# Optimization experiments

Hardware: AMD Instinct MI355X
Metric: run time of the kernel (lower is better)

Reference implementation:

```python
import jax, jax.numpy as jnp
import numpy as np

DEPTH, DIM, HEADS, DIM_HEAD, MLP = 6, 768, 12, 64, 3072
INNER = HEADS * DIM_HEAD  # 768
EPS = 1e-5


def _layernorm(x, w, b):
    m = jnp.mean(x, axis=-1, keepdims=True)
    v = jnp.mean((x - m) ** 2, axis=-1, keepdims=True)
    return (x - m) * jax.lax.rsqrt(v + EPS) * w + b


def setup_inputs() -> dict:
    key = jax.random.key(0)
    ks = jax.random.split(key, 12)
    s = 0.02
    return {
        "x": jax.random.normal(ks[0], (4, 1024, DIM), dtype=jnp.float32),
        "ln1_w": jnp.ones((DEPTH, DIM), jnp.float32),
        "ln1_b": jnp.zeros((DEPTH, DIM), jnp.float32),
        "w_qkv": jax.random.normal(ks[1], (DEPTH, DIM, 3 * INNER), jnp.float32) * s,
        "w_o": jax.random.normal(ks[2], (DEPTH, INNER, DIM), jnp.float32) * s,
        "b_o": jnp.zeros((DEPTH, DIM), jnp.float32),
        "ln2_w": jnp.ones((DEPTH, DIM), jnp.float32),
        "ln2_b": jnp.zeros((DEPTH, DIM), jnp.float32),
        "w1": jax.random.normal(ks[3], (DEPTH, DIM, MLP), jnp.float32) * s,
        "b1": jnp.zeros((DEPTH, MLP), jnp.float32),
        "w2": jax.random.normal(ks[4], (DEPTH, MLP, DIM), jnp.float32) * s,
        "b2": jnp.zeros((DEPTH, DIM), jnp.float32),
    }


def _forward(x, ln1_w, ln1_b, w_qkv, w_o, b_o, ln2_w, ln2_b, w1, b1, w2, b2):
    scale = DIM_HEAD ** -0.5
    b, n, _ = x.shape

    def block(x, p):
        l1w, l1b, wqkv, wo, bo, l2w, l2b, W1, B1, W2, B2 = p
        # --- attention (pre-norm); dropout/droppath are identity in eval ---
        h = _layernorm(x, l1w, l1b)
        qkv = h @ wqkv                                   # [b, n, 3*inner]
        q, k, v = jnp.split(qkv, 3, axis=-1)
        q = q.reshape(b, n, HEADS, DIM_HEAD).transpose(0, 2, 1, 3)
        k = k.reshape(b, n, HEADS, DIM_HEAD).transpose(0, 2, 1, 3)
        v = v.reshape(b, n, HEADS, DIM_HEAD).transpose(0, 2, 1, 3)
        dots = jnp.einsum('bhid,bhjd->bhij', q, k) * scale   # [b, h, n, n]
        attn = jax.nn.softmax(dots, axis=-1)
        out = jnp.einsum('bhij,bhjd->bhid', attn, v)
        out = out.transpose(0, 2, 1, 3).reshape(b, n, INNER)
        x = x + out @ wo + bo
        # --- feed-forward (pre-norm), exact GELU like torch default ---
        h = _layernorm(x, l2w, l2b)
        x = x + jax.nn.gelu(h @ W1 + B1, approximate=False) @ W2 + B2
        return x, None

    x, _ = jax.lax.scan(block, x, (ln1_w, ln1_b, w_qkv, w_o, b_o,
                                   ln2_w, ln2_b, w1, b1, w2, b2))
    return x


def reference(x, ln1_w, ln1_b, w_qkv, w_o, b_o, ln2_w, ln2_b, w1, b1, w2, b2):
    return _forward(x, ln1_w, ln1_b, w_qkv, w_o, b_o, ln2_w, ln2_b, w1, b1, w2, b2)
```

## Files before the change

kernel.cpp:

```cpp
#include <hip/hip_runtime.h>
#include <cmath>
#include <cstdint>

typedef __bf16 bf16_t;
typedef __bf16 bf16x8 __attribute__((ext_vector_type(8)));
typedef __bf16 bf16x4 __attribute__((ext_vector_type(4)));
typedef float  f32x4  __attribute__((ext_vector_type(4)));

#define DEPTH 6
#define DIM   768
#define HEADS 12
#define DH    64
#define MLPD  3072
#define SEQ   1024
#define BATCH 4
#define MTOT  (BATCH*SEQ)
#define QKVN  2304

static __device__ __forceinline__ bf16x8 ld8(const bf16_t* p) {
    return *(const bf16x8*)p;
}

typedef const __attribute__((address_space(1))) unsigned int gas_u32;
typedef __attribute__((address_space(3))) unsigned int las_u32;
static __device__ __forceinline__ void gload16(const bf16_t* g, bf16_t* l) {
    __builtin_amdgcn_global_load_lds((gas_u32*)g, (las_u32*)l, 16, 0, 0);
}

__global__ __launch_bounds__(256) void tcvt_kernel(const float* __restrict__ in,
                                                   bf16_t* __restrict__ out,
                                                   int K, int N) {
    __shared__ float ts[32][33];
    int n0 = blockIdx.x * 32, k0 = blockIdx.y * 32;
    size_t base = (size_t)blockIdx.z * K * N;
    int tx = threadIdx.x & 31, ty = threadIdx.x >> 5;
    #pragma unroll
    for (int r = 0; r < 32; r += 8)
        ts[ty + r][tx] = in[base + (size_t)(k0 + ty + r) * N + n0 + tx];
    __syncthreads();
    #pragma unroll
    for (int r = 0; r < 32; r += 8)
        out[base + (size_t)(n0 + ty + r) * K + k0 + tx] = (bf16_t)ts[tx][ty + r];
}

__global__ __launch_bounds__(256) void lnr_kernel(float* __restrict__ x,
                                                  const float* __restrict__ P,
                                                  int nslices,
                                                  const float* __restrict__ bias,
                                                  const float* __restrict__ w,
                                                  const float* __restrict__ b,
                                                  bf16_t* __restrict__ h,
                                                  int writeLN) {
    int lane = threadIdx.x & 63;
    int row = blockIdx.x * 4 + (threadIdx.x >> 6);
    float4* xr = (float4*)(x + (size_t)row * DIM);
    float4 v0 = xr[lane], v1 = xr[lane + 64], v2 = xr[lane + 128];
    if (nslices) {
        const float4* bi = (const float4*)bias;
        float4 c0 = bi[lane], c1 = bi[lane + 64], c2 = bi[lane + 128];
        v0.x += c0.x; v0.y += c0.y; v0.z += c0.z; v0.w += c0.w;
        v1.x += c1.x; v1.y += c1.y; v1.z += c1.z; v1.w += c1.w;
        v2.x += c2.x; v2.y += c2.y; v2.z += c2.z; v2.w += c2.w;
        for (int s = 0; s < nslices; s++) {
            const float4* pr = (const float4*)(P + (size_t)s * MTOT * DIM
                                                 + (size_t)row * DIM);
            float4 p0 = pr[lane], p1 = pr[lane + 64], p2 = pr[lane + 128];
            v0.x += p0.x; v0.y += p0.y; v0.z += p0.z; v0.w += p0.w;
            v1.x += p1.x; v1.y += p1.y; v1.z += p1.z; v1.w += p1.w;
            v2.x += p2.x; v2.y += p2.y; v2.z += p2.z; v2.w += p2.w;
        }
        xr[lane] = v0; xr[lane + 64] = v1; xr[lane + 128] = v2;
    }
    float s = v0.x + v0.y + v0.z + v0.w + v1.x + v1.y + v1.z + v1.w
            + v2.x + v2.y + v2.z + v2.w;
    float q = v0.x * v0.x + v0.y * v0.y + v0.z * v0.z + v0.w * v0.w
            + v1.x * v1.x + v1.y * v1.y + v1.z * v1.z + v1.w * v1.w
            + v2.x * v2.x + v2.y * v2.y + v2.z * v2.z + v2.w * v2.w;
    #pragma unroll
    for (int off = 32; off > 0; off >>= 1) {
        s += __shfl_xor(s, off);
        q += __shfl_xor(q, off);
    }
    float mean = s * (1.0f / DIM);
    float rstd = rsqrtf(q * (1.0f / DIM) - mean * mean + 1e-5f);
    if (writeLN) {
        const float4* w4 = (const float4*)w;
        const float4* b4 = (const float4*)b;
        bf16_t* hr = h + (size_t)row * DIM;
        float4 vv[3] = {v0, v1, v2};
        #pragma unroll
        for (int k = 0; k < 3; k++) {
            float4 wv = w4[lane + 64 * k], bv = b4[lane + 64 * k];
            bf16x4 o;
            o[0] = (bf16_t)((vv[k].x - mean) * rstd * wv.x + bv.x);
            o[1] = (bf16_t)((vv[k].y - mean) * rstd * wv.y + bv.y);
            o[2] = (bf16_t)((vv[k].z - mean) * rstd * wv.z + bv.z);
            o[3] = (bf16_t)((vv[k].w - mean) * rstd * wv.w + bv.w);
            *(bf16x4*)&hr[(lane + 64 * k) * 4] = o;
        }
    }
}

template <int EPI>
static __device__ __forceinline__ void gemm_body(const bf16_t* __restrict__ A,
                                                 const bf16_t* __restrict__ Bt,
                                                 const float* __restrict__ bias,
                                                 bf16_t* __restrict__ Cb,
                                                 float* __restrict__ Cf,
                                                 bf16_t* __restrict__ Vt,
                                                 int N, int K, int klen) {
    __shared__ __align__(16) bf16_t As[2][256 * 32];
    __shared__ __align__(16) bf16_t Bs[2][64 * 32];
    int t = threadIdx.x;
    int NX = gridDim.x;
    int flat = blockIdx.y * NX + blockIdx.x;
    int jj = flat >> 3;
    int bxs = jj % NX;
    int bys = (flat & 7) + ((jj / NX) << 3);
    int m0 = bys * 256, n0 = bxs * 64;
    int kz = blockIdx.z;
    int kbeg = kz * klen;
    int lane = t & 63, l16 = lane & 15, quad = lane >> 4;
    int wv = t >> 6;
    int wm = wv >> 1, wn = wv & 1;
    f32x4 acc[4][2] = {};

    int sr = lane >> 2;
    int sc = ((lane & 3) ^ ((lane >> 3) & 3)) * 8;
    const bf16_t* gA0 = A  + (size_t)(m0 + wv * 32 + sr) * K + sc;
    const bf16_t* gA1 = gA0 + (size_t)16 * K;
    const bf16_t* gB0 = Bt + (size_t)(n0 + (wv & 3) * 16 + sr) * K + sc;
    bf16_t* lA0 = &As[0][(wv * 32) * 32];
    bf16_t* lA1 = &As[0][(wv * 32 + 16) * 32];
    bf16_t* lB0 = &Bs[0][((wv & 3) * 16) * 32];
    constexpr int bufA = 256 * 32;
    constexpr int bufB = 64 * 32;

    auto stage = [&](int buf, int k0) {
        gload16(gA0 + k0, lA0 + buf * bufA);
        gload16(gA1 + k0, lA1 + buf * bufA);
        if (wv < 4) gload16(gB0 + k0, lB0 + buf * bufB);
    };

    int nIt = klen >> 5;
    stage(0, kbeg);
    int posA = (quad ^ ((l16 >> 1) & 3)) * 8;

    for (int it = 0; it < nIt; it++) {
        __syncthreads();
        if (it + 1 < nIt) stage((it + 1) & 1, kbeg + (it + 1) * 32);
        const bf16_t* as = As[it & 1];
        const bf16_t* bs = Bs[it & 1];
        bf16x8 af[4], bfr[2];
        #pragma unroll
        for (int i = 0; i < 4; i++)
            af[i] = ld8(&as[(wm * 64 + i * 16 + l16) * 32 + posA]);
        #pragma unroll
        for (int j = 0; j < 2; j++)
            bfr[j] = ld8(&bs[(wn * 32 + j * 16 + l16) * 32 + posA]);
        #pragma unroll
        for (int i = 0; i < 4; i++)
            #pragma unroll
            for (int j = 0; j < 2; j++)
                acc[i][j] = __builtin_amdgcn_mfma_f32_16x16x32_bf16(af[i], bfr[j], acc[i][j], 0, 0, 0);
    }

    if constexpr (EPI == 0) {
        if (n0 >= 1536) {
            int b = m0 >> 10;
            #pragma unroll
            for (int i = 0; i < 4; i++) {
                int n = (m0 & 1023) + wm * 64 + i * 16 + quad * 4;
                #pragma unroll
                for (int j = 0; j < 2; j++) {
                    int hc = n0 + wn * 32 + j * 16 + l16 - 1536;
                    int hh = hc >> 6, d = hc & 63;
                    bf16x4 ov;
                    #pragma unroll
                    for (int r = 0; r < 4; r++) ov[r] = (bf16_t)acc[i][j][r];
                    *(bf16x4*)&Vt[(((size_t)b * HEADS + hh) * 64 + d) * SEQ + n] = ov;
                }
            }
            return;
        }
    }
    #pragma unroll
    for (int i = 0; i < 4; i++) {
        int grow = m0 + wm * 64 + i * 16 + quad * 4;
        #pragma unroll
        for (int j = 0; j < 2; j++) {
            int gcol = n0 + wn * 32 + j * 16 + l16;
            float bv = 0.0f;
            if constexpr (EPI == 1) bv = bias[gcol];
            #pragma unroll
            for (int r = 0; r < 4; r++) {
                size_t idx = (size_t)(grow + r) * N + gcol;
                float v = acc[i][j][r];
                if constexpr (EPI == 0) {
                    Cb[idx] = (bf16_t)v;
                } else if constexpr (EPI == 1) {
                    v += bv;
                    v = 0.5f * v * (1.0f + erff(v * 0.70710678118654752f));
                    Cb[idx] = (bf16_t)v;
                } else {
                    Cf[(size_t)kz * MTOT * N + idx] = v;
                }
            }
        }
    }
}

__global__ __launch_bounds__(512) void qkv_gemm(const bf16_t* __restrict__ A,
                                                const bf16_t* __restrict__ Bt,
                                                bf16_t* __restrict__ Cb,
                                                bf16_t* __restrict__ Vt) {
    gemm_body<0>(A, Bt, nullptr, Cb, nullptr, Vt, QKVN, DIM, DIM);
}
__global__ __launch_bounds__(512) void proj_gemm(const bf16_t* __restrict__ A,
                                                 const bf16_t* __restrict__ Bt,
                                                 float* __restrict__ Cf) {
    gemm_body<2>(A, Bt, nullptr, nullptr, Cf, nullptr, DIM, DIM, 384);
}
__global__ __launch_bounds__(512) void mlp1_gemm(const bf16_t* __restrict__ A,
                                                 const bf16_t* __restrict__ Bt,
                                                 const float* __restrict__ bias,
                                                 bf16_t* __restrict__ Cb) {
    gemm_body<1>(A, Bt, bias, Cb, nullptr, nullptr, MLPD, DIM, DIM);
}
__global__ __launch_bounds__(512) void mlp2_gemm(const bf16_t* __restrict__ A,
                                                 const bf16_t* __restrict__ Bt,
                                                 float* __restrict__ Cf) {
    gemm_body<2>(A, Bt, nullptr, nullptr, Cf, nullptr, DIM, MLPD, 768);
}

__global__ __launch_bounds__(256) void attn_kernel(const bf16_t* __restrict__ qkv,
                                                   const bf16_t* __restrict__ vt,
                                                   bf16_t* __restrict__ out) {
    int flat = (blockIdx.z * gridDim.y + blockIdx.y) * gridDim.x + blockIdx.x;
    int jj = flat >> 3;
    int qt = jj & 15;
    int bh = (flat & 7) + ((jj >> 4) << 3);
    int h = bh % HEADS, b = bh / HEADS;
    int t = threadIdx.x;
    int wv = t >> 6, lane = t & 63, l16 = lane & 15, quad = lane >> 4;
    const float LOG2E = 1.44269504f;
    int qw0 = qt * 64 + wv * 16;

    __shared__ __align__(16) bf16_t Ks[2][64 * 64];
    __shared__ __align__(16) bf16_t Vs[2][64 * 64];
    __shared__ __align__(16) bf16_t Pa[4][16 * 72];
    bf16_t* P = Pa[wv];

    size_t bS = (size_t)b * SEQ;
    const bf16_t* qrow = qkv + (bS + qw0 + l16) * QKVN + h * 64;
    bf16x8 qf0 = ld8(qrow + quad * 8);
    bf16x8 qf1 = ld8(qrow + 32 + quad * 8);

    float m = -3e38f, l = 0.0f;
    f32x4 o[4] = {};

    const bf16_t* kbase = qkv + bS * QKVN + 768 + h * 64;
    const bf16_t* vbase = vt + ((size_t)(b * HEADS + h) * 64) * SEQ;

    int ar = lane >> 3;
    int ac = ((lane & 7) ^ ar) * 8;
    int i0 = wv * 2, i1 = wv * 2 + 1;
    const bf16_t* gK0 = kbase + (size_t)(i0 * 8 + ar) * QKVN + ac;
    const bf16_t* gK1 = kbase + (size_t)(i1 * 8 + ar) * QKVN + ac;
    const bf16_t* gV0 = vbase + (size_t)(i0 * 8 + ar) * SEQ + ac;
    const bf16_t* gV1 = vbase + (size_t)(i1 * 8 + ar) * SEQ + ac;

    auto stage = [&](int buf, int kb) {
        gload16(gK0 + (size_t)kb * QKVN, &Ks[buf][i0 * 8 * 64]);
        gload16(gK1 + (size_t)kb * QKVN, &Ks[buf][i1 * 8 * 64]);
        gload16(gV0 + kb, &Vs[buf][i0 * 8 * 64]);
        gload16(gV1 + kb, &Vs[buf][i1 * 8 * 64]);
    };

    stage(0, 0);
    int p0 = (quad ^ (l16 & 7)) * 8;
    int p1 = ((quad + 4) ^ (l16 & 7)) * 8;

    for (int it = 0; it < SEQ / 64; it++) {
        __syncthreads();
        if (it + 1 < SEQ / 64) stage((it + 1) & 1, (it + 1) * 64);
        const bf16_t* ks = Ks[it & 1];
        const bf16_t* vs = Vs[it & 1];

        f32x4 s[4];
        #pragma unroll
        for (int tt = 0; tt < 4; tt++) {
            const bf16_t* kr = &ks[(tt * 16 + l16) * 64];
            f32x4 z = {};
            z = __builtin_amdgcn_mfma_f32_16x16x32_bf16(ld8(kr + p0), qf0, z, 0, 0, 0);
            z = __builtin_amdgcn_mfma_f32_16x16x32_bf16(ld8(kr + p1), qf1, z, 0, 0, 0);
            s[tt] = z;
        }
        float mx = -3e38f;
        #pragma unroll
        for (int tt = 0; tt < 4; tt++)
            #pragma unroll
            for (int r = 0; r < 4; r++) {
                s[tt][r] *= 0.125f;
                mx = fmaxf(mx, s[tt][r]);
            }
        mx = fmaxf(mx, __shfl_xor(mx, 16));
        mx = fmaxf(mx, __shfl_xor(mx, 32));
        float mn = fmaxf(m, mx);
        float alpha = exp2f((m - mn) * LOG2E);
        m = mn;
        float nb = mn * LOG2E;
        float rs = 0.0f;
        #pragma unroll
        for (int tt = 0; tt < 4; tt++) {
            bf16x4 pkt;
            #pragma unroll
            for (int r = 0; r < 4; r++) {
                float p = exp2f(fmaf(s[tt][r], LOG2E, -nb));
                rs += p;
                pkt[r] = (bf16_t)p;
            }
            *(bf16x4*)&P[l16 * 72 + tt * 16 + quad * 4] = pkt;
        }
        l = l * alpha + rs;
        #pragma unroll
        for (int jt = 0; jt < 4; jt++) o[jt] *= alpha;
        asm volatile("s_waitcnt lgkmcnt(0)" ::: "memory");
        bf16x8 pf0 = ld8(&P[l16 * 72 + quad * 8]);
        bf16x8 pf1 = ld8(&P[l16 * 72 + 32 + quad * 8]);
        #pragma unroll
        for (int jt = 0; jt < 4; jt++) {
            const bf16_t* vr = &vs[(jt * 16 + l16) * 64];
            o[jt] = __builtin_amdgcn_mfma_f32_16x16x32_bf16(ld8(vr + p0), pf0, o[jt], 0, 0, 0);
            o[jt] = __builtin_amdgcn_mfma_f32_16x16x32_bf16(ld8(vr + p1), pf1, o[jt], 0, 0, 0);
        }
    }

    l += __shfl_xor(l, 16);
    l += __shfl_xor(l, 32);
    float inv = 1.0f / l;
    bf16_t* orow = out + (bS + qw0 + l16) * DIM + h * 64;
    #pragma unroll
    for (int jt = 0; jt < 4; jt++) {
        bf16x4 ov;
        #pragma unroll
        for (int r = 0; r < 4; r++) ov[r] = (bf16_t)(o[jt][r] * inv);
        *(bf16x4*)&orow[jt * 16 + quad * 4] = ov;
    }
}

extern "C" void kernel_launch(void* const* d_in, const int* in_sizes, int n_in,
                              void* d_out, int out_size, void* d_ws, size_t ws_size,
                              hipStream_t stream) {
    const float* x     = (const float*)d_in[0];
    const float* ln1_w = (const float*)d_in[1];
    const float* ln1_b = (const float*)d_in[2];
    const float* w_qkv = (const float*)d_in[3];
    const float* w_o   = (const float*)d_in[4];
    const float* b_o   = (const float*)d_in[5];
    const float* ln2_w = (const float*)d_in[6];
    const float* ln2_b = (const float*)d_in[7];
    const float* w1    = (const float*)d_in[8];
    const float* b1    = (const float*)d_in[9];
    const float* w2    = (const float*)d_in[10];
    const float* b2    = (const float*)d_in[11];
    float* out = (float*)d_out;

    char* ws = (char*)d_ws;
    size_t off = 0;
    auto alloc = [&](size_t bytes) -> char* {
        char* p = ws + off;
        off += (bytes + 255) & ~(size_t)255;
        return p;
    };
    bf16_t* wqkv_t = (bf16_t*)alloc((size_t)DEPTH * DIM * QKVN * 2);
    bf16_t* wo_t   = (bf16_t*)alloc((size_t)DEPTH * DIM * DIM * 2);
    bf16_t* w1_t   = (bf16_t*)alloc((size_t)DEPTH * DIM * MLPD * 2);
    bf16_t* w2_t   = (bf16_t*)alloc((size_t)DEPTH * MLPD * DIM * 2);
    bf16_t* hbuf   = (bf16_t*)alloc((size_t)MTOT * DIM * 2);
    bf16_t* qkvb   = (bf16_t*)alloc((size_t)MTOT * QKVN * 2);
    bf16_t* vtb    = (bf16_t*)alloc((size_t)BATCH * HEADS * 64 * SEQ * 2);
    bf16_t* aob    = (bf16_t*)alloc((size_t)MTOT * DIM * 2);
    bf16_t* midb   = (bf16_t*)alloc((size_t)MTOT * MLPD * 2);
    float*  Pm     = (float*)alloc((size_t)4 * MTOT * DIM * 4);
    float*  Pp     = (float*)qkvb;
    if (off > ws_size) return;

    tcvt_kernel<<<dim3(QKVN / 32, DIM / 32, DEPTH), 256, 0, stream>>>(w_qkv, wqkv_t, DIM, QKVN);
    tcvt_kernel<<<dim3(DIM / 32,  DIM / 32, DEPTH), 256, 0, stream>>>(w_o,   wo_t,   DIM, DIM);
    tcvt_kernel<<<dim3(MLPD / 32, DIM / 32, DEPTH), 256, 0, stream>>>(w1,    w1_t,   DIM, MLPD);
    tcvt_kernel<<<dim3(DIM / 32, MLPD / 32, DEPTH), 256, 0, stream>>>(w2,    w2_t,   MLPD, DIM);

    hipMemcpyAsync(out, x, (size_t)MTOT * DIM * 4, hipMemcpyDeviceToDevice, stream);

    lnr_kernel<<<MTOT / 4, 256, 0, stream>>>(out, nullptr, 0, nullptr,
                                             ln1_w, ln1_b, hbuf, 1);

    for (int L = 0; L < DEPTH; L++) {
        qkv_gemm<<<dim3(QKVN / 64, MTOT / 256, 1), 512, 0, stream>>>(
            hbuf, wqkv_t + (size_t)L * DIM * QKVN, qkvb, vtb);
        attn_kernel<<<dim3(SEQ / 64, HEADS, BATCH), 256, 0, stream>>>(qkvb, vtb, aob);
        proj_gemm<<<dim3(DIM / 64, MTOT / 256, 2), 512, 0, stream>>>(
            aob, wo_t + (size_t)L * DIM * DIM, Pp);
        lnr_kernel<<<MTOT / 4, 256, 0, stream>>>(out, Pp, 2, b_o + L * DIM,
                                                 ln2_w + L * DIM, ln2_b + L * DIM,
                                                 hbuf, 1);
        mlp1_gemm<<<dim3(MLPD / 64, MTOT / 256, 1), 512, 0, stream>>>(
            hbuf, w1_t + (size_t)L * DIM * MLPD, b1 + L * MLPD, midb);
        mlp2_gemm<<<dim3(DIM / 64, MTOT / 256, 4), 512, 0, stream>>>(
            midb, w2_t + (size_t)L * MLPD * DIM, Pm);
        if (L < DEPTH - 1) {
            lnr_kernel<<<MTOT / 4, 256, 0, stream>>>(out, Pm, 4, b2 + L * DIM,
                                                     ln1_w + (L + 1) * DIM,
                                                     ln1_b + (L + 1) * DIM, hbuf, 1);
        } else {
            lnr_kernel<<<MTOT / 4, 256, 0, stream>>>(out, Pm, 4, b2 + L * DIM,
                                                     nullptr, nullptr, nullptr, 0);
        }
    }
}
```

Baseline: 1.291 ms.

## Retile GEMMs to 128x64 blocks with 64-wide K stage and 4 waves

The shared GEMM body moves from 256x64 tiles with 8 waves and a K step of 32 to 128x64 tiles with 4 waves and a K step of 64. Each wave now does two MFMA sub-steps per barrier, and the LDS XOR swizzle is redone for 64-element rows. The aim is to halve the number of barriers and global-load rounds per K, double the block count, and lower per-block LDS and thread count so more blocks fit per CU. In exchange, each block reuses less data across M, so more global traffic goes to re-reading B.

```diff
diff --git a/kernel.cpp b/kernel.cpp
--- a/kernel.cpp
+++ b/kernel.cpp
@@ -109,15 +109,15 @@
                                                  float* __restrict__ Cf,
                                                  bf16_t* __restrict__ Vt,
                                                  int N, int K, int klen) {
-    __shared__ __align__(16) bf16_t As[2][256 * 32];
-    __shared__ __align__(16) bf16_t Bs[2][64 * 32];
+    __shared__ __align__(16) bf16_t As[2][128 * 64];
+    __shared__ __align__(16) bf16_t Bs[2][64 * 64];
     int t = threadIdx.x;
     int NX = gridDim.x;
     int flat = blockIdx.y * NX + blockIdx.x;
     int jj = flat >> 3;
     int bxs = jj % NX;
     int bys = (flat & 7) + ((jj / NX) << 3);
-    int m0 = bys * 256, n0 = bxs * 64;
+    int m0 = bys * 128, n0 = bxs * 64;
     int kz = blockIdx.z;
     int kbeg = kz * klen;
     int lane = t & 63, l16 = lane & 15, quad = lane >> 4;
@@ -125,44 +125,49 @@
     int wm = wv >> 1, wn = wv & 1;
     f32x4 acc[4][2] = {};
 
-    int sr = lane >> 2;
-    int sc = ((lane & 3) ^ ((lane >> 3) & 3)) * 8;
-    const bf16_t* gA0 = A  + (size_t)(m0 + wv * 32 + sr) * K + sc;
-    const bf16_t* gA1 = gA0 + (size_t)16 * K;
-    const bf16_t* gB0 = Bt + (size_t)(n0 + (wv & 3) * 16 + sr) * K + sc;
-    bf16_t* lA0 = &As[0][(wv * 32) * 32];
-    bf16_t* lA1 = &As[0][(wv * 32 + 16) * 32];
-    bf16_t* lB0 = &Bs[0][((wv & 3) * 16) * 32];
-    constexpr int bufA = 256 * 32;
-    constexpr int bufB = 64 * 32;
+    int ar = lane >> 3;
+    int ac = ((lane & 7) ^ ar) * 8;
+    const bf16_t* gA = A  + (size_t)(m0 + wv * 32 + ar) * K + ac;
+    const bf16_t* gB = Bt + (size_t)(n0 + wv * 16 + ar) * K + ac;
+    bf16_t* lA = &As[0][(wv * 32) * 64];
+    bf16_t* lB = &Bs[0][(wv * 16) * 64];
+    constexpr int bufA = 128 * 64;
+    constexpr int bufB = 64 * 64;
 
     auto stage = [&](int buf, int k0) {
-        gload16(gA0 + k0, lA0 + buf * bufA);
-        gload16(gA1 + k0, lA1 + buf * bufA);
-        if (wv < 4) gload16(gB0 + k0, lB0 + buf * bufB);
+        #pragma unroll
+        for (int i = 0; i < 4; i++)
+            gload16(gA + (size_t)(i * 8) * K + k0, lA + buf * bufA + i * 8 * 64);
+        #pragma unroll
+        for (int i = 0; i < 2; i++)
+            gload16(gB + (size_t)(i * 8) * K + k0, lB + buf * bufB + i * 8 * 64);
     };
 
-    int nIt = klen >> 5;
+    int nIt = klen >> 6;
     stage(0, kbeg);
-    int posA = (quad ^ ((l16 >> 1) & 3)) * 8;
+    int rk = l16 & 7;
 
     for (int it = 0; it < nIt; it++) {
         __syncthreads();
-        if (it + 1 < nIt) stage((it + 1) & 1, kbeg + (it + 1) * 32);
+        if (it + 1 < nIt) stage((it + 1) & 1, kbeg + (it + 1) * 64);
         const bf16_t* as = As[it & 1];
         const bf16_t* bs = Bs[it & 1];
-        bf16x8 af[4], bfr[2];
-        #pragma unroll
-        for (int i = 0; i < 4; i++)
-            af[i] = ld8(&as[(wm * 64 + i * 16 + l16) * 32 + posA]);
-        #pragma unroll
-        for (int j = 0; j < 2; j++)
-            bfr[j] = ld8(&bs[(wn * 32 + j * 16 + l16) * 32 + posA]);
-        #pragma unroll
-        for (int i = 0; i < 4; i++)
+        #pragma unroll
+        for (int kk = 0; kk < 2; kk++) {
+            int pos = ((kk * 4 + quad) ^ rk) * 8;
+            bf16x8 af[4], bfr[2];
+            #pragma unroll
+            for (int i = 0; i < 4; i++)
+                af[i] = ld8(&as[(wm * 64 + i * 16 + l16) * 64 + pos]);
             #pragma unroll
             for (int j = 0; j < 2; j++)
-                acc[i][j] = __builtin_amdgcn_mfma_f32_16x16x32_bf16(af[i], bfr[j], acc[i][j], 0, 0, 0);
+                bfr[j] = ld8(&bs[(wn * 32 + j * 16 + l16) * 64 + pos]);
+            #pragma unroll
+            for (int i = 0; i < 4; i++)
+                #pragma unroll
+                for (int j = 0; j < 2; j++)
+                    acc[i][j] = __builtin_amdgcn_mfma_f32_16x16x32_bf16(af[i], bfr[j], acc[i][j], 0, 0, 0);
+        }
     }
 
     if constexpr (EPI == 0) {
@@ -210,24 +215,24 @@
     }
 }
 
-__global__ __launch_bounds__(512) void qkv_gemm(const bf16_t* __restrict__ A,
+__global__ __launch_bounds__(256) void qkv_gemm(const bf16_t* __restrict__ A,
                                                 const bf16_t* __restrict__ Bt,
                                                 bf16_t* __restrict__ Cb,
                                                 bf16_t* __restrict__ Vt) {
     gemm_body<0>(A, Bt, nullptr, Cb, nullptr, Vt, QKVN, DIM, DIM);
 }
-__global__ __launch_bounds__(512) void proj_gemm(const bf16_t* __restrict__ A,
+__global__ __launch_bounds__(256) void proj_gemm(const bf16_t* __restrict__ A,
                                                  const bf16_t* __restrict__ Bt,
                                                  float* __restrict__ Cf) {
     gemm_body<2>(A, Bt, nullptr, nullptr, Cf, nullptr, DIM, DIM, 384);
 }
-__global__ __launch_bounds__(512) void mlp1_gemm(const bf16_t* __restrict__ A,
+__global__ __launch_bounds__(256) void mlp1_gemm(const bf16_t* __restrict__ A,
                                                  const bf16_t* __restrict__ Bt,
                                                  const float* __restrict__ bias,
                                                  bf16_t* __restrict__ Cb) {
     gemm_body<1>(A, Bt, bias, Cb, nullptr, nullptr, MLPD, DIM, DIM);
 }
-__global__ __launch_bounds__(512) void mlp2_gemm(const bf16_t* __restrict__ A,
+__global__ __launch_bounds__(256) void mlp2_gemm(const bf16_t* __restrict__ A,
                                                  const bf16_t* __restrict__ Bt,
                                                  float* __restrict__ Cf) {
     gemm_body<2>(A, Bt, nullptr, nullptr, Cf, nullptr, DIM, MLPD, 768);
@@ -397,17 +402,17 @@
                                              ln1_w, ln1_b, hbuf, 1);
 
     for (int L = 0; L < DEPTH; L++) {
-        qkv_gemm<<<dim3(QKVN / 64, MTOT / 256, 1), 512, 0, stream>>>(
+        qkv_gemm<<<dim3(QKVN / 64, MTOT / 128, 1), 256, 0, stream>>>(
             hbuf, wqkv_t + (size_t)L * DIM * QKVN, qkvb, vtb);
         attn_kernel<<<dim3(SEQ / 64, HEADS, BATCH), 256, 0, stream>>>(qkvb, vtb, aob);
-        proj_gemm<<<dim3(DIM / 64, MTOT / 256, 2), 512, 0, stream>>>(
+        proj_gemm<<<dim3(DIM / 64, MTOT / 128, 2), 256, 0, stream>>>(
             aob, wo_t + (size_t)L * DIM * DIM, Pp);
         lnr_kernel<<<MTOT / 4, 256, 0, stream>>>(out, Pp, 2, b_o + L * DIM,
                                                  ln2_w + L * DIM, ln2_b + L * DIM,
                                                  hbuf, 1);
-        mlp1_gemm<<<dim3(MLPD / 64, MTOT / 256, 1), 512, 0, stream>>>(
+        mlp1_gemm<<<dim3(MLPD / 64, MTOT / 128, 1), 256, 0, stream>>>(
             hbuf, w1_t + (size_t)L * DIM * MLPD, b1 + L * MLPD, midb);
-        mlp2_gemm<<<dim3(DIM / 64, MTOT / 256, 4), 512, 0, stream>>>(
+        mlp2_gemm<<<dim3(DIM / 64, MTOT / 128, 4), 256, 0, stream>>>(
             midb, w2_t + (size_t)L * MLPD * DIM, Pm);
         if (L < DEPTH - 1) {
             lnr_kernel<<<MTOT / 4, 256, 0, stream>>>(out, Pm, 4, b2 + L * DIM,
```

Measured after the change: 1.256 ms. 2.7% less time.
